# Kernel optimization log

Measured on AMD Instinct MI355X. Metric: run time of the kernel, lower is better.

The kernel has to match this reference:

```python
import jax, jax.numpy as jnp
import numpy as np


def floor_ste(x):
    # forward: floor(x); backward: identity (straight-through estimator)
    return x + jax.lax.stop_gradient(jnp.floor(x) - x)


def _int_polynomial(x_int, sf):
    c0, c1, c2 = 0.35815147, 0.96963238, 1.0
    b_int = floor_ste((c1 / c0) / sf)
    c_int = floor_ste((c2 / c0) / (sf * sf))
    z = x_int * (x_int + b_int) + c_int
    return z, c0 * sf * sf


def _int_exp(x_int, sf):
    x0 = -0.69314718
    n = 15
    x0_int = floor_ste(x0 / sf)
    x_int = jnp.maximum(x_int, n * x0_int)
    q = floor_ste(x_int / x0_int)
    r = x_int - x0_int * q
    exp_int, exp_sf = _int_polynomial(r, sf)
    exp_int = jnp.maximum(floor_ste(exp_int * jnp.exp2(n - q)), 0.0)
    return exp_int, exp_sf / (2.0 ** n)


def _int_softmax(x, sf):
    x_int = x / sf
    x_int = x_int - jnp.max(x_int, axis=-1, keepdims=True)
    exp_int, exp_sf = _int_exp(x_int, sf)
    exp_int_sum = jnp.sum(exp_int, axis=-1, keepdims=True)
    return exp_int, exp_int_sum, exp_sf


def setup_inputs() -> dict:
    key = jax.random.key(0)
    k1, = jax.random.split(key, 1)
    x = jax.random.normal(k1, (2, 16, 1024, 1024), dtype=jnp.float32)
    scale = jnp.float32(0.05)          # activation quantization step
    threshold = jnp.array([0.1], dtype=jnp.float32)  # nn.Parameter init
    return {"x": x, "scale": scale, "threshold": threshold}


def reference(x, scale, threshold):
    output_bit = 8
    threshold_bits = 8
    exp_int, exp_int_sum, exp_sf = _int_softmax(x, scale)
    factor = floor_ste((2.0 ** 32) / exp_int_sum)
    out_scale_A = threshold / (2.0 ** output_bit - 1.0)   # shape [1]
    out_scale_B = 1.0 / (2.0 ** output_bit - 1.0)
    approx_threshold = (floor_ste(threshold * 2.0 ** threshold_bits)
                        * exp_int_sum / (2.0 ** threshold_bits))
    mask_A = exp_int <= approx_threshold
    exp_int_A = jnp.where(mask_A, exp_int, 0.0)
    exp_int_B = jnp.where(mask_A, 0.0, exp_int)
    softmax_int_A = floor_ste(exp_int_A * factor / ((2.0 ** 32) * out_scale_A))
    softmax_int_B = floor_ste(exp_int_B * factor / ((2.0 ** 32) * out_scale_B))
    softmax_int_B = jnp.minimum(softmax_int_B, 255.0)
    return softmax_int_A * out_scale_A + softmax_int_B * out_scale_B
```

## Files before the change

kernel.cpp:

```cpp
#include <hip/hip_runtime.h>
#include <math.h>

#pragma clang fp contract(off)

#define TPB 256
#define ROWLEN 1024

__global__ __launch_bounds__(TPB) void qsplit_int_softmax_kernel(
    const float* __restrict__ x,
    const float* __restrict__ scale_p,
    const float* __restrict__ thr_p,
    float* __restrict__ out)
{
    const int lane = threadIdx.x & 63;
    const int wid  = threadIdx.x >> 6;
    const int row  = blockIdx.x * 4 + wid;
    const size_t rbase = (size_t)row * ROWLEN + (size_t)lane * 4;

    const float  sf   = scale_p[0];
    const float  thr  = thr_p[0];
    const double sfd  = (double)sf;
    const double rsfd = 1.0 / sfd;

    const double x0d    = floor(-0.69314718 / sfd);
    const float  x0f    = (float)x0d;
    const float  bfc    = (float)floor((0.96963238 / 0.35815147) / sfd);
    const float  cfc    = (float)floor((1.0 / 0.35815147) / (sfd * sfd));
    const float  clampf = (float)(15.0 * x0d);
    const float  invx0f = 1.0f / x0f;

    float4 xv[4];
    #pragma unroll
    for (int k = 0; k < 4; ++k)
        xv[k] = *(const float4*)(x + rbase + (size_t)k * 256);

    float xi[16];
    #pragma unroll
    for (int k = 0; k < 4; ++k) {
        xi[k*4+0] = (float)((double)xv[k].x * rsfd);
        xi[k*4+1] = (float)((double)xv[k].y * rsfd);
        xi[k*4+2] = (float)((double)xv[k].z * rsfd);
        xi[k*4+3] = (float)((double)xv[k].w * rsfd);
    }

    float m = xi[0];
    #pragma unroll
    for (int j = 1; j < 16; ++j) m = fmaxf(m, xi[j]);
    #pragma unroll
    for (int off = 1; off < 64; off <<= 1)
        m = fmaxf(m, __shfl_xor(m, off));

    float e[16];
    double lsum = 0.0;
    #pragma unroll
    for (int j = 0; j < 16; ++j) {
        float v = xi[j] - m;
        v = fmaxf(v, clampf);
        float qf = floorf(v * invx0f);
        int   ki = 15 - (int)qf;
        float r  = v - x0f * qf;
        float t  = r + bfc;
        float z  = r * t + cfc;
        float ei = floorf(ldexpf(z, ki));
        ei = fmaxf(ei, 0.0f);
        e[j] = ei;
        lsum += (double)ei;
    }

    #pragma unroll
    for (int off = 1; off < 64; off <<= 1)
        lsum += __shfl_xor(lsum, off);
    const double s = lsum;

    const double factor_d = floor(4294967296.0 / s);
    const float  fac_f = (float)factor_d;
    const double ath   = (floor((double)thr * 256.0) * s) * (1.0 / 256.0);

    const float  osA  = thr / 255.0f;
    const float  osB  = 1.0f / 255.0f;
    const float  denA = 4294967296.0f * osA;
    const float  denB = 4294967296.0f * osB;
    const double invA = 1.0 / (double)denA;
    const double invB = 1.0 / (double)denB;

    #pragma unroll
    for (int k = 0; k < 4; ++k) {
        float res[4];
        #pragma unroll
        for (int jj = 0; jj < 4; ++jj) {
            const float ei  = e[k*4+jj];
            const bool  isA = ((double)ei <= ath);
            const float numer = ei * fac_f;
            const double inv  = isA ? invA : invB;
            const float  qf2  = (float)((double)numer * inv);
            float si = floorf(qf2);
            si = fminf(si, isA ? 3.0e38f : 255.0f);
            res[jj] = si * (isA ? osA : osB);
        }
        float4 o; o.x = res[0]; o.y = res[1]; o.z = res[2]; o.w = res[3];
        *(float4*)(out + rbase + (size_t)k * 256) = o;
    }
}

extern "C" void kernel_launch(void* const* d_in, const int* in_sizes, int n_in,
                              void* d_out, int out_size, void* d_ws, size_t ws_size,
                              hipStream_t stream) {
    const float* x     = (const float*)d_in[0];
    const float* scale = (const float*)d_in[1];
    const float* thr   = (const float*)d_in[2];
    float* out = (float*)d_out;

    const int total = in_sizes[0];
    const int rows  = total / ROWLEN;
    const int blocks = rows / 4;

    qsplit_int_softmax_kernel<<<dim3(blocks), dim3(TPB), 0, stream>>>(
        x, scale, thr, out);
}
```

Baseline: 231.6 us.

## Replace fp64 math with fp32 and double-float tricks, add nontemporal stores

Replaces the per-element fp64 multiply for x/scale with a double-float (hi/lo) fp32 FMA product, and accumulates the row sum as 32-bit integers reduced as a 64-bit integer instead of doubles. The threshold compare and final scaling now use fp32 in place of fp64 conversions, and output stores become nontemporal. This removes slow fp64 work on MI355X, where FP64 vector throughput is lower than FP32. It risks off-by-one floor differences from the rounding changes in the final scaling and threshold compare.

```diff
diff --git a/kernel.cpp b/kernel.cpp
--- a/kernel.cpp
+++ b/kernel.cpp
@@ -5,6 +5,8 @@
 
 #define TPB 256
 #define ROWLEN 1024
+
+typedef float f32x4 __attribute__((ext_vector_type(4)));
 
 __global__ __launch_bounds__(TPB) void qsplit_int_softmax_kernel(
     const float* __restrict__ x,
@@ -17,30 +19,36 @@
     const int row  = blockIdx.x * 4 + wid;
     const size_t rbase = (size_t)row * ROWLEN + (size_t)lane * 4;
 
-    const float  sf   = scale_p[0];
-    const float  thr  = thr_p[0];
+    const float sf  = scale_p[0];
+    const float thr = thr_p[0];
+
     const double sfd  = (double)sf;
-    const double rsfd = 1.0 / sfd;
+    const double rd   = 1.0 / sfd;
+    const float  rh   = (float)rd;
+    const float  rl   = (float)(rd - (double)rh);
 
     const double x0d    = floor(-0.69314718 / sfd);
     const float  x0f    = (float)x0d;
     const float  bfc    = (float)floor((0.96963238 / 0.35815147) / sfd);
     const float  cfc    = (float)floor((1.0 / 0.35815147) / (sfd * sfd));
     const float  clampf = (float)(15.0 * x0d);
-    const float  invx0f = 1.0f / x0f;
+    const float  invx0f = (float)(1.0 / x0d);
 
-    float4 xv[4];
+    f32x4 xv[4];
     #pragma unroll
     for (int k = 0; k < 4; ++k)
-        xv[k] = *(const float4*)(x + rbase + (size_t)k * 256);
+        xv[k] = *(const f32x4*)(x + rbase + (size_t)k * 256);
 
     float xi[16];
     #pragma unroll
     for (int k = 0; k < 4; ++k) {
-        xi[k*4+0] = (float)((double)xv[k].x * rsfd);
-        xi[k*4+1] = (float)((double)xv[k].y * rsfd);
-        xi[k*4+2] = (float)((double)xv[k].z * rsfd);
-        xi[k*4+3] = (float)((double)xv[k].w * rsfd);
+        #pragma unroll
+        for (int jj = 0; jj < 4; ++jj) {
+            const float xx = xv[k][jj];
+            const float p  = xx * rh;
+            const float e  = __builtin_fmaf(xx, rh, -p);
+            xi[k*4+jj]     = p + __builtin_fmaf(xx, rl, e);
+        }
     }
 
     float m = xi[0];
@@ -50,55 +58,52 @@
     for (int off = 1; off < 64; off <<= 1)
         m = fmaxf(m, __shfl_xor(m, off));
 
-    float e[16];
-    double lsum = 0.0;
+    float e16[16];
+    unsigned int usum = 0;
     #pragma unroll
     for (int j = 0; j < 16; ++j) {
         float v = xi[j] - m;
         v = fmaxf(v, clampf);
-        float qf = floorf(v * invx0f);
-        int   ki = 15 - (int)qf;
-        float r  = v - x0f * qf;
-        float t  = r + bfc;
-        float z  = r * t + cfc;
-        float ei = floorf(ldexpf(z, ki));
+        const float qf = floorf(v * invx0f);
+        const int   qi = (int)qf;
+        const float r  = v - x0f * qf;
+        const float t  = r + bfc;
+        const float z  = r * t + cfc;
+        float ei = floorf(ldexpf(z, 15 - qi));
         ei = fmaxf(ei, 0.0f);
-        e[j] = ei;
-        lsum += (double)ei;
+        e16[j] = ei;
+        usum += (unsigned int)ei;
     }
 
+    unsigned long long ws = usum;
     #pragma unroll
     for (int off = 1; off < 64; off <<= 1)
-        lsum += __shfl_xor(lsum, off);
-    const double s = lsum;
+        ws += __shfl_xor(ws, off);
+    const double s = (double)ws;
 
     const double factor_d = floor(4294967296.0 / s);
     const float  fac_f = (float)factor_d;
-    const double ath   = (floor((double)thr * 256.0) * s) * (1.0 / 256.0);
+    const float  ath_f = (float)((floor((double)thr * 256.0) * s) * (1.0 / 256.0));
 
     const float  osA  = thr / 255.0f;
     const float  osB  = 1.0f / 255.0f;
-    const float  denA = 4294967296.0f * osA;
-    const float  denB = 4294967296.0f * osB;
-    const double invA = 1.0 / (double)denA;
-    const double invB = 1.0 / (double)denB;
+    const float  invA = (float)(1.0 / (4294967296.0 * (double)osA));
+    const float  invB = (float)(1.0 / (4294967296.0 * (double)osB));
 
     #pragma unroll
     for (int k = 0; k < 4; ++k) {
-        float res[4];
+        f32x4 o;
         #pragma unroll
         for (int jj = 0; jj < 4; ++jj) {
-            const float ei  = e[k*4+jj];
-            const bool  isA = ((double)ei <= ath);
-            const float numer = ei * fac_f;
-            const double inv  = isA ? invA : invB;
-            const float  qf2  = (float)((double)numer * inv);
-            float si = floorf(qf2);
+            const float ei  = e16[k*4+jj];
+            const bool  isA = (ei <= ath_f);
+            const float t1  = ei * fac_f;
+            const float t2  = t1 * (isA ? invA : invB);
+            float si = floorf(t2);
             si = fminf(si, isA ? 3.0e38f : 255.0f);
-            res[jj] = si * (isA ? osA : osB);
+            o[jj] = si * (isA ? osA : osB);
         }
-        float4 o; o.x = res[0]; o.y = res[1]; o.z = res[2]; o.w = res[3];
-        *(float4*)(out + rbase + (size_t)k * 256) = o;
+        __builtin_nontemporal_store(o, (f32x4*)(out + rbase + (size_t)k * 256));
     }
 }
 
```

New measurement: 232.0 us. About the same (+0.2%).
